# Kernel optimization log

Measured on AMD Instinct MI355X. Metric: run time of the kernel, lower is better.

Reference implementation:

```python
import jax, jax.numpy as jnp
import numpy as np

B = 65536        # batch of (Z, N) token pairs
V = 512          # vocab size per input
D = 1024         # hidden_dim == embedding_dim
IN = 2 * D       # input_dim = embedding_dim * len(vocab_size)
E = 4            # num_experts (hardcoded in MoEModel)
OUT = 128        # output_dim


def setup_inputs() -> dict:
    key = jax.random.key(0)
    ks = jax.random.split(key, 6)
    x = jax.random.randint(ks[0], (B, 2), 0, V, dtype=jnp.int64)
    emb0 = jax.random.normal(ks[1], (V, D), dtype=jnp.float32)
    emb1 = jax.random.normal(ks[2], (V, D), dtype=jnp.float32)
    W1 = jax.random.normal(ks[3], (E, IN, D), dtype=jnp.float32) * 0.02
    b1 = jnp.zeros((E, D), dtype=jnp.float32)
    W2 = jax.random.normal(ks[4], (E, D, OUT), dtype=jnp.float32) * 0.02
    b2 = jnp.zeros((E, OUT), dtype=jnp.float32)
    Wg = jax.random.normal(ks[5], (IN, E), dtype=jnp.float32) * 0.02
    bg = jnp.zeros((E,), dtype=jnp.float32)
    return {"x": x, "emb0": emb0, "emb1": emb1, "W1": W1, "b1": b1,
            "W2": W2, "b2": b2, "Wg": Wg, "bg": bg}


def reference(x, emb0, emb1, W1, b1, W2, b2, Wg, bg):
    # embed_input: gather each column's embedding and concat -> [B, IN]
    e = jnp.concatenate([emb0[x[:, 0]], emb1[x[:, 1]]], axis=1)
    # gating network: softmax(MuReadout(e)) -> [B, E]
    gates = jax.nn.softmax(e @ Wg + bg, axis=-1)
    # all 4 experts run densely: Linear -> SiLU -> MuReadout, batched over E
    h = jax.nn.silu(jnp.einsum('bi,eid->bed', e, W1) + b1)      # [B, E, D]
    expert_out = jnp.einsum('bed,edo->beo', h, W2) + b2          # [B, E, OUT]
    # einsum('ij,ikj->ik') combine: softmax-weighted mixture over experts
    out = jnp.einsum('be,beo->bo', gates, expert_out)            # [B, OUT]
    return out
```

## Files before the change

### kernel.cpp

```cpp
#include <hip/hip_runtime.h>


#define NTOK 65536

typedef __attribute__((ext_vector_type(8))) short short8;
typedef __attribute__((ext_vector_type(4))) float f32x4;

__device__ __forceinline__ unsigned short f2b(float f) {
  unsigned int u = __builtin_bit_cast(unsigned int, f);
  u += 0x7fffu + ((u >> 16) & 1u);
  return (unsigned short)(u >> 16);
}
__device__ __forceinline__ float bflo(unsigned int u) {
  return __builtin_bit_cast(float, u << 16);
}
__device__ __forceinline__ float bfhi(unsigned int u) {
  return __builtin_bit_cast(float, u & 0xffff0000u);
}

__global__ void prep_g(const float* __restrict__ emb0, const float* __restrict__ emb1,
                       const float* __restrict__ Wg, const float* __restrict__ bg,
                       float* __restrict__ G0, float* __restrict__ G1) {
  const int bid = blockIdx.x;
  const int half = bid >> 9;
  const int v = bid & 511;
  const float* __restrict__ emb = half ? emb1 : emb0;
  const float* __restrict__ wg = Wg + (size_t)half * 1024 * 4;
  float a0 = 0.f, a1 = 0.f, a2 = 0.f, a3 = 0.f;
  for (int i = threadIdx.x; i < 1024; i += 256) {
    const float ev = emb[(size_t)v * 1024 + i];
    const float4 w = *(const float4*)(wg + (size_t)i * 4);
    a0 += ev * w.x; a1 += ev * w.y; a2 += ev * w.z; a3 += ev * w.w;
  }
  __shared__ float red[4][256];
  red[0][threadIdx.x] = a0; red[1][threadIdx.x] = a1;
  red[2][threadIdx.x] = a2; red[3][threadIdx.x] = a3;
  __syncthreads();
  for (int s = 128; s > 0; s >>= 1) {
    if (threadIdx.x < s) {
      red[0][threadIdx.x] += red[0][threadIdx.x + s];
      red[1][threadIdx.x] += red[1][threadIdx.x + s];
      red[2][threadIdx.x] += red[2][threadIdx.x + s];
      red[3][threadIdx.x] += red[3][threadIdx.x + s];
    }
    __syncthreads();
  }
  if (threadIdx.x < 4) {
    const float val = red[threadIdx.x][0] + (half == 0 ? bg[threadIdx.x] : 0.f);
    (half ? G1 : G0)[(size_t)v * 4 + threadIdx.x] = val;
  }
}

__global__ void prep_w2(const float* __restrict__ W2, unsigned short* __restrict__ W2T) {
  __shared__ float st[64][65];
  const int kt = blockIdx.x;
  const int ot = blockIdx.y;
  const int tid = threadIdx.x;
  for (int it = 0; it < 16; ++it) {
    const int idx = it * 256 + tid;
    const int k = idx >> 6, o = idx & 63;
    st[k][o] = W2[(size_t)(kt * 64 + k) * 128 + ot * 64 + o];
  }
  __syncthreads();
  for (int it = 0; it < 4; ++it) {
    const int idx = it * 256 + tid;
    const int o = idx >> 4, c = idx & 15;
    const unsigned int p0 =
        (unsigned int)f2b(st[c * 4 + 0][o]) | ((unsigned int)f2b(st[c * 4 + 1][o]) << 16);
    const unsigned int p1 =
        (unsigned int)f2b(st[c * 4 + 2][o]) | ((unsigned int)f2b(st[c * 4 + 3][o]) << 16);
    *(uint2*)(W2T + (size_t)(ot * 64 + o) * 4096 + kt * 64 + c * 4) = make_uint2(p0, p1);
  }
}

__launch_bounds__(256, 2)
__global__ void build_tables(const float* __restrict__ emb0, const float* __restrict__ emb1,
                             const float* __restrict__ W1, const float* __restrict__ b1,
                             unsigned short* __restrict__ T0, unsigned short* __restrict__ T1) {
  const int z = blockIdx.y;
  const int e = z >> 1, half = z & 1;
  const int vt = blockIdx.x >> 3;
  const int dt = blockIdx.x & 7;
  const float* __restrict__ embA = half ? emb1 : emb0;
  const float* __restrict__ W = W1 + ((size_t)e * 2048 + (size_t)half * 1024) * 1024;
  unsigned short* __restrict__ Tout = (half ? T1 : T0) + (size_t)e * 512 * 1024;

  __shared__ unsigned short Atile[128 * 64];
  __shared__ unsigned short Btile[128 * 64];

  const int tid = threadIdx.x, lane = tid & 63, wave = tid >> 6;
  const int wm = wave >> 1, wn = wave & 1;

  f32x4 acc[4][4] = {};

  const int arow = tid >> 3, ac = tid & 7;
  int awoff[4];
#pragma unroll
  for (int q = 0; q < 4; ++q) {
    const int r = arow + 32 * q;
    awoff[q] = r * 128 + ((ac * 16) ^ ((r & 7) << 4));
  }
  const int lh16 = (lane >> 4) * 16;
  int aoff[4], asw[4], boff[4], bsw[4];
#pragma unroll
  for (int i = 0; i < 4; ++i) {
    const int ra = wm * 64 + i * 16 + (lane & 15);
    aoff[i] = ra * 128; asw[i] = (ra & 7) << 4;
    const int rb = wn * 64 + i * 16 + (lane & 15);
    boff[i] = rb * 128; bsw[i] = (rb & 7) << 4;
  }

  for (int kt = 0; kt < 16; ++kt) {
    const int k0 = kt * 64;
    __syncthreads();
#pragma unroll
    for (int q = 0; q < 4; ++q) {
      const float* src = embA + (size_t)(vt * 128 + arow + 32 * q) * 1024 + k0 + ac * 8;
      const float4 lo = *(const float4*)src;
      const float4 hi = *(const float4*)(src + 4);
      short8 o;
      o[0] = (short)f2b(lo.x); o[1] = (short)f2b(lo.y);
      o[2] = (short)f2b(lo.z); o[3] = (short)f2b(lo.w);
      o[4] = (short)f2b(hi.x); o[5] = (short)f2b(hi.y);
      o[6] = (short)f2b(hi.z); o[7] = (short)f2b(hi.w);
      *(short8*)((char*)Atile + awoff[q]) = o;
    }
#pragma unroll
    for (int q = 0; q < 4; ++q) {
      const int dd = arow + 32 * q;
      const float* wsrc = W + (size_t)(k0 + ac * 8) * 1024 + dt * 128 + dd;
      short8 o;
#pragma unroll
      for (int j = 0; j < 8; ++j) o[j] = (short)f2b(wsrc[(size_t)j * 1024]);
      *(short8*)((char*)Btile + awoff[q]) = o;
    }
    __syncthreads();
    const char* Ab = (const char*)Atile;
    const char* Bb = (const char*)Btile;
#pragma unroll
    for (int kk = 0; kk < 2; ++kk) {
      const int kb = kk * 64 + lh16;
      short8 af[4], bfr[4];
#pragma unroll
      for (int mi = 0; mi < 4; ++mi) af[mi] = *(const short8*)(Ab + aoff[mi] + (kb ^ asw[mi]));
#pragma unroll
      for (int ni = 0; ni < 4; ++ni) bfr[ni] = *(const short8*)(Bb + boff[ni] + (kb ^ bsw[ni]));
#pragma unroll
      for (int mi = 0; mi < 4; ++mi)
#pragma unroll
        for (int ni = 0; ni < 4; ++ni)
          acc[mi][ni] = __builtin_amdgcn_mfma_f32_16x16x32_bf16(af[mi], bfr[ni], acc[mi][ni], 0, 0, 0);
    }
  }
  const float* bb = b1 + (size_t)e * 1024;
#pragma unroll
  for (int ni = 0; ni < 4; ++ni) {
    const int dcol = dt * 128 + wn * 64 + ni * 16 + (lane & 15);
    const float bias = (half == 0) ? bb[dcol] : 0.f;
#pragma unroll
    for (int mi = 0; mi < 4; ++mi) {
      const int vrow0 = vt * 128 + wm * 64 + mi * 16 + ((lane >> 4) << 2);
      const f32x4 a = acc[mi][ni];
#pragma unroll
      for (int j = 0; j < 4; ++j)
        Tout[(size_t)(vrow0 + j) * 1024 + dcol] = f2b(a[j] + bias);
    }
  }
}

__launch_bounds__(256, 2)
__global__ void moe_main(const int* __restrict__ X,
                         const unsigned short* __restrict__ T0,
                         const unsigned short* __restrict__ T1,
                         const unsigned short* __restrict__ W2T,
                         const float* __restrict__ G0,
                         const float* __restrict__ G1,
                         const float* __restrict__ b2v,
                         float* __restrict__ out) {
  __shared__ unsigned short Atile[2][128 * 64];
  __shared__ unsigned short Btile[2][128 * 64];
  __shared__ float gl[128 * 4];
  __shared__ int xs0[128], xs1[128];

  const int tid = threadIdx.x, lane = tid & 63, wave = tid >> 6;
  const int wm = wave >> 1, wn = wave & 1;
  const int b0 = blockIdx.x * 128;

  if (tid < 128) {
    const int b = b0 + tid;
    const int x0 = X[2 * b], x1 = X[2 * b + 1];
    xs0[tid] = x0; xs1[tid] = x1;
    const float4 l0 = *(const float4*)(G0 + 4 * x0);
    const float4 l1 = *(const float4*)(G1 + 4 * x1);
    const float z0 = l0.x + l1.x, z1 = l0.y + l1.y;
    const float z2 = l0.z + l1.z, z3 = l0.w + l1.w;
    const float m = fmaxf(fmaxf(z0, z1), fmaxf(z2, z3));
    const float e0 = __expf(z0 - m), e1 = __expf(z1 - m);
    const float e2 = __expf(z2 - m), e3 = __expf(z3 - m);
    const float inv = __builtin_amdgcn_rcpf(e0 + e1 + e2 + e3);
    *(float4*)(&gl[4 * tid]) = make_float4(e0 * inv, e1 * inv, e2 * inv, e3 * inv);
  }
  __syncthreads();

  const int arow = tid >> 3, ac = tid & 7;
  int xr0[4], xr1[4], awoff[4];
  float4 gr[4];
#pragma unroll
  for (int q = 0; q < 4; ++q) {
    const int r = arow + 32 * q;
    xr0[q] = xs0[r]; xr1[q] = xs1[r];
    gr[q] = *(const float4*)(&gl[4 * r]);
    awoff[q] = r * 128 + ((ac * 16) ^ ((r & 7) << 4));
  }

  const int lh16 = (lane >> 4) * 16;
  int aoff[4], asw[4], boff[4], bsw[4];
#pragma unroll
  for (int i = 0; i < 4; ++i) {
    const int ra = wm * 64 + i * 16 + (lane & 15);
    aoff[i] = ra * 128; asw[i] = (ra & 7) << 4;
    const int rb = wn * 64 + i * 16 + (lane & 15);
    boff[i] = rb * 128; bsw[i] = (rb & 7) << 4;
  }

  f32x4 acc[4][4] = {};
  uint4 bw[4], ua[4], ub[4];
  float gen[4];

  auto loadNext = [&](int tt) {
    const int e = tt >> 4, d0 = (tt & 15) << 6;
#pragma unroll
    for (int q = 0; q < 4; ++q) {
      const int o = arow + 32 * q;
      bw[q] = *(const uint4*)(W2T + (size_t)o * 4096 + tt * 64 + ac * 8);
      ua[q] = *(const uint4*)(T0 + (((size_t)(e * 512 + xr0[q])) << 10) + d0 + ac * 8);
      ub[q] = *(const uint4*)(T1 + (((size_t)(e * 512 + xr1[q])) << 10) + d0 + ac * 8);
      gen[q] = (e == 0) ? gr[q].x : (e == 1) ? gr[q].y : (e == 2) ? gr[q].z : gr[q].w;
    }
  };
  auto writeNext = [&](int bi) {
    char* An = (char*)Atile[bi];
    char* Bn = (char*)Btile[bi];
#pragma unroll
    for (int q = 0; q < 4; ++q) {
      *(uint4*)(Bn + awoff[q]) = bw[q];
      const float g = gen[q];
      float f[8];
      f[0] = bflo(ua[q].x) + bflo(ub[q].x);
      f[1] = bfhi(ua[q].x) + bfhi(ub[q].x);
      f[2] = bflo(ua[q].y) + bflo(ub[q].y);
      f[3] = bfhi(ua[q].y) + bfhi(ub[q].y);
      f[4] = bflo(ua[q].z) + bflo(ub[q].z);
      f[5] = bfhi(ua[q].z) + bfhi(ub[q].z);
      f[6] = bflo(ua[q].w) + bflo(ub[q].w);
      f[7] = bfhi(ua[q].w) + bfhi(ub[q].w);
      short8 o8;
#pragma unroll
      for (int i = 0; i < 8; ++i) {
        const float tv = f[i];
        const float sg = g * tv * __builtin_amdgcn_rcpf(1.f + __expf(-tv));
        o8[i] = (short)f2b(sg);
      }
      *(short8*)(An + awoff[q]) = o8;
    }
  };

  loadNext(0);
  writeNext(0);
  __syncthreads();

  for (int t = 0; t < 64; ++t) {
    const int buf = t & 1;
    if (t < 63) loadNext(t + 1);
    const char* Ab = (const char*)Atile[buf];
    const char* Bb = (const char*)Btile[buf];
#pragma unroll
    for (int kk = 0; kk < 2; ++kk) {
      const int kb = kk * 64 + lh16;
      short8 af[4], bfr[4];
#pragma unroll
      for (int mi = 0; mi < 4; ++mi) af[mi] = *(const short8*)(Ab + aoff[mi] + (kb ^ asw[mi]));
#pragma unroll
      for (int ni = 0; ni < 4; ++ni) bfr[ni] = *(const short8*)(Bb + boff[ni] + (kb ^ bsw[ni]));
#pragma unroll
      for (int mi = 0; mi < 4; ++mi)
#pragma unroll
        for (int ni = 0; ni < 4; ++ni)
          acc[mi][ni] = __builtin_amdgcn_mfma_f32_16x16x32_bf16(af[mi], bfr[ni], acc[mi][ni], 0, 0, 0);
    }
    if (t < 63) writeNext(buf ^ 1);
    __syncthreads();
  }

#pragma unroll
  for (int ni = 0; ni < 4; ++ni) {
    const int col = wn * 64 + ni * 16 + (lane & 15);
    const float c0 = b2v[col], c1 = b2v[128 + col];
    const float c2 = b2v[256 + col], c3 = b2v[384 + col];
#pragma unroll
    for (int mi = 0; mi < 4; ++mi) {
      const int row0 = wm * 64 + mi * 16 + ((lane >> 4) << 2);
      const f32x4 a = acc[mi][ni];
#pragma unroll
      for (int j = 0; j < 4; ++j) {
        const int row = row0 + j;
        const float4 g = *(const float4*)(&gl[4 * row]);
        out[(size_t)(b0 + row) * 128 + col] = a[j] + g.x * c0 + g.y * c1 + g.z * c2 + g.w * c3;
      }
    }
  }
}

extern "C" void kernel_launch(void* const* d_in, const int* in_sizes, int n_in,
                              void* d_out, int out_size, void* d_ws, size_t ws_size,
                              hipStream_t stream) {
  const int*   X    = (const int*)  d_in[0];
  const float* emb0 = (const float*)d_in[1];
  const float* emb1 = (const float*)d_in[2];
  const float* W1   = (const float*)d_in[3];
  const float* b1   = (const float*)d_in[4];
  const float* W2   = (const float*)d_in[5];
  const float* b2   = (const float*)d_in[6];
  const float* Wg   = (const float*)d_in[7];
  const float* bg   = (const float*)d_in[8];
  float* out = (float*)d_out;

  char* ws = (char*)d_ws;
  unsigned short* T0  = (unsigned short*)(ws);
  unsigned short* T1  = (unsigned short*)(ws + (size_t)4 * 1024 * 1024);
  unsigned short* W2T = (unsigned short*)(ws + (size_t)8 * 1024 * 1024);
  float* G0 = (float*)(ws + (size_t)9 * 1024 * 1024);
  float* G1 = (float*)(ws + (size_t)9 * 1024 * 1024 + 8192);

  hipLaunchKernelGGL(prep_w2, dim3(64, 2), dim3(256), 0, stream, W2, W2T);
  hipLaunchKernelGGL(prep_g, dim3(1024), dim3(256), 0, stream, emb0, emb1, Wg, bg, G0, G1);
  hipLaunchKernelGGL(build_tables, dim3(32, 8), dim3(256), 0, stream, emb0, emb1, W1, b1, T0, T1);
  hipLaunchKernelGGL(moe_main, dim3(512), dim3(256), 0, stream, X, T0, T1, W2T, G0, G1, b2, out);
}
```

Measured before the change: 371.6 us.

## Pre-convert W1 and embeddings to bf16, restructure table build and main kernel

New prep kernels convert the embeddings to bf16 and transpose W1 to bf16 once. build_tables can then load both operands as contiguous 16-byte vectors, replacing the strided fp32 gathers and per-element conversion, and it now uses 64-wide output tiles over 512 blocks with a register prefetch. moe_main moves to 512-thread blocks with single-buffered LDS plus a register prefetch, a custom barrier macro, and a swizzled block-index mapping meant to improve cache locality. The cost is two extra kernel launches and extra workspace traffic, and the single LDS buffer exposes more barrier stalls.

```diff
diff --git a/kernel.cpp b/kernel.cpp
--- a/kernel.cpp
+++ b/kernel.cpp
@@ -1,22 +1,23 @@
 #include <hip/hip_runtime.h>
 
-
-#define NTOK 65536
 
 typedef __attribute__((ext_vector_type(8))) short short8;
 typedef __attribute__((ext_vector_type(4))) float f32x4;
 
-__device__ __forceinline__ unsigned short f2b(float f) {
+static __device__ __forceinline__ unsigned short f2b(float f) {
   unsigned int u = __builtin_bit_cast(unsigned int, f);
   u += 0x7fffu + ((u >> 16) & 1u);
   return (unsigned short)(u >> 16);
 }
-__device__ __forceinline__ float bflo(unsigned int u) {
+static __device__ __forceinline__ float bflo(unsigned int u) {
   return __builtin_bit_cast(float, u << 16);
 }
-__device__ __forceinline__ float bfhi(unsigned int u) {
+static __device__ __forceinline__ float bfhi(unsigned int u) {
   return __builtin_bit_cast(float, u & 0xffff0000u);
 }
+
+#define BARRIER() do { asm volatile("s_waitcnt lgkmcnt(0)" ::: "memory"); \
+                       __builtin_amdgcn_s_barrier(); } while (0)
 
 __global__ void prep_g(const float* __restrict__ emb0, const float* __restrict__ emb1,
                        const float* __restrict__ Wg, const float* __restrict__ bg,
@@ -53,8 +54,7 @@
 
 __global__ void prep_w2(const float* __restrict__ W2, unsigned short* __restrict__ W2T) {
   __shared__ float st[64][65];
-  const int kt = blockIdx.x;
-  const int ot = blockIdx.y;
+  const int kt = blockIdx.x, ot = blockIdx.y;
   const int tid = threadIdx.x;
   for (int it = 0; it < 16; ++it) {
     const int idx = it * 256 + tid;
@@ -73,89 +73,135 @@
   }
 }
 
+__global__ void prep_emb(const float* __restrict__ emb0, const float* __restrict__ emb1,
+                         unsigned short* __restrict__ E0, unsigned short* __restrict__ E1) {
+  const float* __restrict__ src = blockIdx.y ? emb1 : emb0;
+  unsigned short* __restrict__ dst = blockIdx.y ? E1 : E0;
+  const size_t base = (size_t)blockIdx.x * 2048 + (size_t)threadIdx.x * 8;
+  const float4 lo = *(const float4*)(src + base);
+  const float4 hi = *(const float4*)(src + base + 4);
+  short8 o;
+  o[0] = (short)f2b(lo.x); o[1] = (short)f2b(lo.y);
+  o[2] = (short)f2b(lo.z); o[3] = (short)f2b(lo.w);
+  o[4] = (short)f2b(hi.x); o[5] = (short)f2b(hi.y);
+  o[6] = (short)f2b(hi.z); o[7] = (short)f2b(hi.w);
+  *(short8*)(dst + base) = o;
+}
+
+__global__ void prep_w1t(const float* __restrict__ W1, unsigned short* __restrict__ W1T) {
+  __shared__ float st[64][65];
+  const int z = blockIdx.y;
+  const int kt = blockIdx.x >> 4, dt = blockIdx.x & 15;
+  const int e = z >> 1, half = z & 1;
+  const int tid = threadIdx.x;
+  const int r = tid >> 2, cg = (tid & 3) * 16;
+  const float* src = W1 + ((size_t)e * 2048 + half * 1024 + kt * 64 + r) * 1024 + dt * 64 + cg;
+#pragma unroll
+  for (int j = 0; j < 4; ++j) {
+    const float4 v = *(const float4*)(src + j * 4);
+    st[r][cg + j * 4 + 0] = v.x; st[r][cg + j * 4 + 1] = v.y;
+    st[r][cg + j * 4 + 2] = v.z; st[r][cg + j * 4 + 3] = v.w;
+  }
+  __syncthreads();
+  const int dr = tid >> 2, kb = (tid & 3) * 16;
+  short8 o0, o1;
+#pragma unroll
+  for (int m = 0; m < 8; ++m) o0[m] = (short)f2b(st[kb + m][dr]);
+#pragma unroll
+  for (int m = 0; m < 8; ++m) o1[m] = (short)f2b(st[kb + 8 + m][dr]);
+  unsigned short* dst = W1T + ((size_t)z * 1024 + dt * 64 + dr) * 1024 + kt * 64 + kb;
+  *(short8*)dst = o0;
+  *(short8*)(dst + 8) = o1;
+}
+
 __launch_bounds__(256, 2)
-__global__ void build_tables(const float* __restrict__ emb0, const float* __restrict__ emb1,
-                             const float* __restrict__ W1, const float* __restrict__ b1,
+__global__ void build_tables(const unsigned short* __restrict__ E0,
+                             const unsigned short* __restrict__ E1,
+                             const unsigned short* __restrict__ W1T,
+                             const float* __restrict__ b1,
                              unsigned short* __restrict__ T0, unsigned short* __restrict__ T1) {
-  const int z = blockIdx.y;
+  __shared__ unsigned short At[128 * 64];
+  __shared__ unsigned short Bt[64 * 64];
+
+  const int bid = blockIdx.x;
+  const int z = bid >> 6, rem = bid & 63;
+  const int vt = rem >> 4, dt = rem & 15;
   const int e = z >> 1, half = z & 1;
-  const int vt = blockIdx.x >> 3;
-  const int dt = blockIdx.x & 7;
-  const float* __restrict__ embA = half ? emb1 : emb0;
-  const float* __restrict__ W = W1 + ((size_t)e * 2048 + (size_t)half * 1024) * 1024;
+  const unsigned short* __restrict__ E = half ? E1 : E0;
+  const unsigned short* __restrict__ Wp = W1T + (size_t)z * 1024 * 1024;
   unsigned short* __restrict__ Tout = (half ? T1 : T0) + (size_t)e * 512 * 1024;
-
-  __shared__ unsigned short Atile[128 * 64];
-  __shared__ unsigned short Btile[128 * 64];
 
   const int tid = threadIdx.x, lane = tid & 63, wave = tid >> 6;
   const int wm = wave >> 1, wn = wave & 1;
 
-  f32x4 acc[4][4] = {};
-
-  const int arow = tid >> 3, ac = tid & 7;
-  int awoff[4];
-#pragma unroll
-  for (int q = 0; q < 4; ++q) {
-    const int r = arow + 32 * q;
-    awoff[q] = r * 128 + ((ac * 16) ^ ((r & 7) << 4));
-  }
-  const int lh16 = (lane >> 4) * 16;
-  int aoff[4], asw[4], boff[4], bsw[4];
-#pragma unroll
-  for (int i = 0; i < 4; ++i) {
-    const int ra = wm * 64 + i * 16 + (lane & 15);
-    aoff[i] = ra * 128; asw[i] = (ra & 7) << 4;
-    const int rb = wn * 64 + i * 16 + (lane & 15);
-    boff[i] = rb * 128; bsw[i] = (rb & 7) << 4;
-  }
-
-  for (int kt = 0; kt < 16; ++kt) {
-    const int k0 = kt * 64;
-    __syncthreads();
-#pragma unroll
-    for (int q = 0; q < 4; ++q) {
-      const float* src = embA + (size_t)(vt * 128 + arow + 32 * q) * 1024 + k0 + ac * 8;
-      const float4 lo = *(const float4*)src;
-      const float4 hi = *(const float4*)(src + 4);
-      short8 o;
-      o[0] = (short)f2b(lo.x); o[1] = (short)f2b(lo.y);
-      o[2] = (short)f2b(lo.z); o[3] = (short)f2b(lo.w);
-      o[4] = (short)f2b(hi.x); o[5] = (short)f2b(hi.y);
-      o[6] = (short)f2b(hi.z); o[7] = (short)f2b(hi.w);
-      *(short8*)((char*)Atile + awoff[q]) = o;
-    }
-#pragma unroll
-    for (int q = 0; q < 4; ++q) {
-      const int dd = arow + 32 * q;
-      const float* wsrc = W + (size_t)(k0 + ac * 8) * 1024 + dt * 128 + dd;
-      short8 o;
-#pragma unroll
-      for (int j = 0; j < 8; ++j) o[j] = (short)f2b(wsrc[(size_t)j * 1024]);
-      *(short8*)((char*)Btile + awoff[q]) = o;
-    }
-    __syncthreads();
-    const char* Ab = (const char*)Atile;
-    const char* Bb = (const char*)Btile;
+  const int arow = tid >> 1, ah = tid & 1;
+  int wAoff[4];
+#pragma unroll
+  for (int i = 0; i < 4; ++i)
+    wAoff[i] = arow * 128 + ((ah * 64 + i * 16) ^ ((arow & 7) << 4));
+  const int bcol = tid >> 2, bc = tid & 3;
+  int wBoff[2];
+#pragma unroll
+  for (int i = 0; i < 2; ++i)
+    wBoff[i] = bcol * 128 + ((bc * 32 + i * 16) ^ ((bcol & 7) << 4));
+
+  const unsigned short* aSrc = E + (size_t)(vt * 128 + arow) * 1024 + ah * 32;
+  const unsigned short* bSrc = Wp + (size_t)(dt * 64 + bcol) * 1024 + bc * 16;
+
+  const int kq = (lane >> 4) * 16;
+  int rAoff[4], rAsw[4], rBoff[2], rBsw[2];
+#pragma unroll
+  for (int mi = 0; mi < 4; ++mi) {
+    const int ra = wm * 64 + mi * 16 + (lane & 15);
+    rAoff[mi] = ra * 128; rAsw[mi] = (ra & 7) << 4;
+  }
+#pragma unroll
+  for (int ni = 0; ni < 2; ++ni) {
+    const int cb = wn * 32 + ni * 16 + (lane & 15);
+    rBoff[ni] = cb * 128; rBsw[ni] = (cb & 7) << 4;
+  }
+
+  f32x4 acc[4][2] = {};
+  uint4 ea[4]; uint4 eb[2];
+
+  auto issueLoads = [&](int kt2) {
+    const int k0 = kt2 * 64;
+#pragma unroll
+    for (int i = 0; i < 4; ++i) ea[i] = *(const uint4*)(aSrc + k0 + i * 8);
+#pragma unroll
+    for (int i = 0; i < 2; ++i) eb[i] = *(const uint4*)(bSrc + k0 + i * 8);
+  };
+
+  issueLoads(0);
+  for (int kt2 = 0; kt2 < 16; ++kt2) {
+    BARRIER();
+#pragma unroll
+    for (int i = 0; i < 4; ++i) *(uint4*)((char*)At + wAoff[i]) = ea[i];
+#pragma unroll
+    for (int i = 0; i < 2; ++i) *(uint4*)((char*)Bt + wBoff[i]) = eb[i];
+    if (kt2 < 15) issueLoads(kt2 + 1);
+    BARRIER();
 #pragma unroll
     for (int kk = 0; kk < 2; ++kk) {
-      const int kb = kk * 64 + lh16;
-      short8 af[4], bfr[4];
-#pragma unroll
-      for (int mi = 0; mi < 4; ++mi) af[mi] = *(const short8*)(Ab + aoff[mi] + (kb ^ asw[mi]));
-#pragma unroll
-      for (int ni = 0; ni < 4; ++ni) bfr[ni] = *(const short8*)(Bb + boff[ni] + (kb ^ bsw[ni]));
+      const int kb = kk * 64 + kq;
+      short8 af[4], bfr[2];
 #pragma unroll
       for (int mi = 0; mi < 4; ++mi)
-#pragma unroll
-        for (int ni = 0; ni < 4; ++ni)
+        af[mi] = *(const short8*)((char*)At + rAoff[mi] + (kb ^ rAsw[mi]));
+#pragma unroll
+      for (int ni = 0; ni < 2; ++ni)
+        bfr[ni] = *(const short8*)((char*)Bt + rBoff[ni] + (kb ^ rBsw[ni]));
+#pragma unroll
+      for (int mi = 0; mi < 4; ++mi)
+#pragma unroll
+        for (int ni = 0; ni < 2; ++ni)
           acc[mi][ni] = __builtin_amdgcn_mfma_f32_16x16x32_bf16(af[mi], bfr[ni], acc[mi][ni], 0, 0, 0);
     }
   }
   const float* bb = b1 + (size_t)e * 1024;
 #pragma unroll
-  for (int ni = 0; ni < 4; ++ni) {
-    const int dcol = dt * 128 + wn * 64 + ni * 16 + (lane & 15);
+  for (int ni = 0; ni < 2; ++ni) {
+    const int dcol = dt * 64 + wn * 32 + ni * 16 + (lane & 15);
     const float bias = (half == 0) ? bb[dcol] : 0.f;
 #pragma unroll
     for (int mi = 0; mi < 4; ++mi) {
@@ -168,7 +214,7 @@
   }
 }
 
-__launch_bounds__(256, 2)
+__launch_bounds__(512, 4)
 __global__ void moe_main(const int* __restrict__ X,
                          const unsigned short* __restrict__ T0,
                          const unsigned short* __restrict__ T1,
@@ -177,14 +223,16 @@
                          const float* __restrict__ G1,
                          const float* __restrict__ b2v,
                          float* __restrict__ out) {
-  __shared__ unsigned short Atile[2][128 * 64];
-  __shared__ unsigned short Btile[2][128 * 64];
+  __shared__ unsigned short At[128 * 64];
+  __shared__ unsigned short Bt[128 * 64];
   __shared__ float gl[128 * 4];
   __shared__ int xs0[128], xs1[128];
 
   const int tid = threadIdx.x, lane = tid & 63, wave = tid >> 6;
   const int wm = wave >> 1, wn = wave & 1;
-  const int b0 = blockIdx.x * 128;
+  int bid = blockIdx.x;
+  bid = (bid & 7) * 64 + (bid >> 3);
+  const int b0 = bid * 128;
 
   if (tid < 128) {
     const int b = b0 + tid;
@@ -202,94 +250,88 @@
   }
   __syncthreads();
 
-  const int arow = tid >> 3, ac = tid & 7;
-  int xr0[4], xr1[4], awoff[4];
-  float4 gr[4];
-#pragma unroll
-  for (int q = 0; q < 4; ++q) {
-    const int r = arow + 32 * q;
-    xr0[q] = xs0[r]; xr1[q] = xs1[r];
-    gr[q] = *(const float4*)(&gl[4 * r]);
-    awoff[q] = r * 128 + ((ac * 16) ^ ((r & 7) << 4));
-  }
-
-  const int lh16 = (lane >> 4) * 16;
-  int aoff[4], asw[4], boff[4], bsw[4];
-#pragma unroll
-  for (int i = 0; i < 4; ++i) {
-    const int ra = wm * 64 + i * 16 + (lane & 15);
-    aoff[i] = ra * 128; asw[i] = (ra & 7) << 4;
-    const int rb = wn * 64 + i * 16 + (lane & 15);
-    boff[i] = rb * 128; bsw[i] = (rb & 7) << 4;
-  }
-
-  f32x4 acc[4][4] = {};
-  uint4 bw[4], ua[4], ub[4];
-  float gen[4];
-
-  auto loadNext = [&](int tt) {
-    const int e = tt >> 4, d0 = (tt & 15) << 6;
-#pragma unroll
-    for (int q = 0; q < 4; ++q) {
-      const int o = arow + 32 * q;
-      bw[q] = *(const uint4*)(W2T + (size_t)o * 4096 + tt * 64 + ac * 8);
-      ua[q] = *(const uint4*)(T0 + (((size_t)(e * 512 + xr0[q])) << 10) + d0 + ac * 8);
-      ub[q] = *(const uint4*)(T1 + (((size_t)(e * 512 + xr1[q])) << 10) + d0 + ac * 8);
-      gen[q] = (e == 0) ? gr[q].x : (e == 1) ? gr[q].y : (e == 2) ? gr[q].z : gr[q].w;
-    }
+  const int arow = tid >> 2, ac = tid & 3;
+  const int sx0 = xs0[arow], sx1 = xs1[arow];
+  const float4 grow = *(const float4*)(&gl[4 * arow]);
+  int wOff[2];
+#pragma unroll
+  for (int i = 0; i < 2; ++i)
+    wOff[i] = arow * 128 + ((ac * 32 + i * 16) ^ ((arow & 7) << 4));
+
+  const int kq = (lane >> 4) * 16;
+  int rAoff[2], rAsw[2], rBoff[4], rBsw[4];
+#pragma unroll
+  for (int mi = 0; mi < 2; ++mi) {
+    const int ra = wm * 32 + mi * 16 + (lane & 15);
+    rAoff[mi] = ra * 128; rAsw[mi] = (ra & 7) << 4;
+  }
+#pragma unroll
+  for (int ni = 0; ni < 4; ++ni) {
+    const int cb = wn * 64 + ni * 16 + (lane & 15);
+    rBoff[ni] = cb * 128; rBsw[ni] = (cb & 7) << 4;
+  }
+
+  f32x4 acc[2][4] = {};
+  uint4 ua[2], ub[2], bw[2];
+
+  auto issueLoads = [&](int t) {
+    const int e = t >> 4, d0 = (t & 15) << 6;
+    const unsigned short* p0 = T0 + (((size_t)(e * 512 + sx0)) << 10) + d0 + ac * 16;
+    const unsigned short* p1 = T1 + (((size_t)(e * 512 + sx1)) << 10) + d0 + ac * 16;
+    const unsigned short* pb = W2T + (size_t)arow * 4096 + t * 64 + ac * 16;
+    ua[0] = *(const uint4*)p0; ua[1] = *(const uint4*)(p0 + 8);
+    ub[0] = *(const uint4*)p1; ub[1] = *(const uint4*)(p1 + 8);
+    bw[0] = *(const uint4*)pb; bw[1] = *(const uint4*)(pb + 8);
   };
-  auto writeNext = [&](int bi) {
-    char* An = (char*)Atile[bi];
-    char* Bn = (char*)Btile[bi];
-#pragma unroll
-    for (int q = 0; q < 4; ++q) {
-      *(uint4*)(Bn + awoff[q]) = bw[q];
-      const float g = gen[q];
+
+  issueLoads(0);
+  for (int t = 0; t < 64; ++t) {
+    const int e = t >> 4;
+    const float g = (e == 0) ? grow.x : (e == 1) ? grow.y : (e == 2) ? grow.z : grow.w;
+    short8 sa[2];
+#pragma unroll
+    for (int i = 0; i < 2; ++i) {
       float f[8];
-      f[0] = bflo(ua[q].x) + bflo(ub[q].x);
-      f[1] = bfhi(ua[q].x) + bfhi(ub[q].x);
-      f[2] = bflo(ua[q].y) + bflo(ub[q].y);
-      f[3] = bfhi(ua[q].y) + bfhi(ub[q].y);
-      f[4] = bflo(ua[q].z) + bflo(ub[q].z);
-      f[5] = bfhi(ua[q].z) + bfhi(ub[q].z);
-      f[6] = bflo(ua[q].w) + bflo(ub[q].w);
-      f[7] = bfhi(ua[q].w) + bfhi(ub[q].w);
+      f[0] = bflo(ua[i].x) + bflo(ub[i].x);
+      f[1] = bfhi(ua[i].x) + bfhi(ub[i].x);
+      f[2] = bflo(ua[i].y) + bflo(ub[i].y);
+      f[3] = bfhi(ua[i].y) + bfhi(ub[i].y);
+      f[4] = bflo(ua[i].z) + bflo(ub[i].z);
+      f[5] = bfhi(ua[i].z) + bfhi(ub[i].z);
+      f[6] = bflo(ua[i].w) + bflo(ub[i].w);
+      f[7] = bfhi(ua[i].w) + bfhi(ub[i].w);
       short8 o8;
 #pragma unroll
-      for (int i = 0; i < 8; ++i) {
-        const float tv = f[i];
+      for (int j = 0; j < 8; ++j) {
+        const float tv = f[j];
         const float sg = g * tv * __builtin_amdgcn_rcpf(1.f + __expf(-tv));
-        o8[i] = (short)f2b(sg);
+        o8[j] = (short)f2b(sg);
       }
-      *(short8*)(An + awoff[q]) = o8;
-    }
-  };
-
-  loadNext(0);
-  writeNext(0);
-  __syncthreads();
-
-  for (int t = 0; t < 64; ++t) {
-    const int buf = t & 1;
-    if (t < 63) loadNext(t + 1);
-    const char* Ab = (const char*)Atile[buf];
-    const char* Bb = (const char*)Btile[buf];
+      sa[i] = o8;
+    }
+    BARRIER();
+    *(uint4*)((char*)At + wOff[0]) = *(uint4*)&sa[0];
+    *(uint4*)((char*)At + wOff[1]) = *(uint4*)&sa[1];
+    *(uint4*)((char*)Bt + wOff[0]) = bw[0];
+    *(uint4*)((char*)Bt + wOff[1]) = bw[1];
+    if (t < 63) issueLoads(t + 1);
+    BARRIER();
 #pragma unroll
     for (int kk = 0; kk < 2; ++kk) {
-      const int kb = kk * 64 + lh16;
-      short8 af[4], bfr[4];
-#pragma unroll
-      for (int mi = 0; mi < 4; ++mi) af[mi] = *(const short8*)(Ab + aoff[mi] + (kb ^ asw[mi]));
-#pragma unroll
-      for (int ni = 0; ni < 4; ++ni) bfr[ni] = *(const short8*)(Bb + boff[ni] + (kb ^ bsw[ni]));
-#pragma unroll
-      for (int mi = 0; mi < 4; ++mi)
+      const int kb = kk * 64 + kq;
+      short8 af[2], bfr[4];
+#pragma unroll
+      for (int mi = 0; mi < 2; ++mi)
+        af[mi] = *(const short8*)((char*)At + rAoff[mi] + (kb ^ rAsw[mi]));
+#pragma unroll
+      for (int ni = 0; ni < 4; ++ni)
+        bfr[ni] = *(const short8*)((char*)Bt + rBoff[ni] + (kb ^ rBsw[ni]));
+#pragma unroll
+      for (int mi = 0; mi < 2; ++mi)
 #pragma unroll
         for (int ni = 0; ni < 4; ++ni)
           acc[mi][ni] = __builtin_amdgcn_mfma_f32_16x16x32_bf16(af[mi], bfr[ni], acc[mi][ni], 0, 0, 0);
     }
-    if (t < 63) writeNext(buf ^ 1);
-    __syncthreads();
   }
 
 #pragma unroll
@@ -298,8 +340,8 @@
     const float c0 = b2v[col], c1 = b2v[128 + col];
     const float c2 = b2v[256 + col], c3 = b2v[384 + col];
 #pragma unroll
-    for (int mi = 0; mi < 4; ++mi) {
-      const int row0 = wm * 64 + mi * 16 + ((lane >> 4) << 2);
+    for (int mi = 0; mi < 2; ++mi) {
+      const int row0 = wm * 32 + mi * 16 + ((lane >> 4) << 2);
       const f32x4 a = acc[mi][ni];
 #pragma unroll
       for (int j = 0; j < 4; ++j) {
@@ -326,14 +368,20 @@
   float* out = (float*)d_out;
 
   char* ws = (char*)d_ws;
+  const size_t MB = 1024 * 1024;
   unsigned short* T0  = (unsigned short*)(ws);
-  unsigned short* T1  = (unsigned short*)(ws + (size_t)4 * 1024 * 1024);
-  unsigned short* W2T = (unsigned short*)(ws + (size_t)8 * 1024 * 1024);
-  float* G0 = (float*)(ws + (size_t)9 * 1024 * 1024);
-  float* G1 = (float*)(ws + (size_t)9 * 1024 * 1024 + 8192);
-
+  unsigned short* T1  = (unsigned short*)(ws + 4 * MB);
+  unsigned short* W2T = (unsigned short*)(ws + 8 * MB);
+  float* G0 = (float*)(ws + 9 * MB);
+  float* G1 = (float*)(ws + 9 * MB + 8192);
+  unsigned short* E0  = (unsigned short*)(ws + 10 * MB);
+  unsigned short* E1  = (unsigned short*)(ws + 11 * MB);
+  unsigned short* W1T = (unsigned short*)(ws + 12 * MB);
+
+  hipLaunchKernelGGL(prep_emb, dim3(256, 2), dim3(256), 0, stream, emb0, emb1, E0, E1);
+  hipLaunchKernelGGL(prep_w1t, dim3(256, 8), dim3(256), 0, stream, W1, W1T);
   hipLaunchKernelGGL(prep_w2, dim3(64, 2), dim3(256), 0, stream, W2, W2T);
   hipLaunchKernelGGL(prep_g, dim3(1024), dim3(256), 0, stream, emb0, emb1, Wg, bg, G0, G1);
-  hipLaunchKernelGGL(build_tables, dim3(32, 8), dim3(256), 0, stream, emb0, emb1, W1, b1, T0, T1);
-  hipLaunchKernelGGL(moe_main, dim3(512), dim3(256), 0, stream, X, T0, T1, W2T, G0, G1, b2, out);
-}
+  hipLaunchKernelGGL(build_tables, dim3(512), dim3(256), 0, stream, E0, E1, W1T, b1, T0, T1);
+  hipLaunchKernelGGL(moe_main, dim3(512), dim3(512), 0, stream, X, T0, T1, W2T, G0, G1, b2, out);
+}
```

After: 346.0 us. 6.9% less time.
